# Kernel optimization log

Measured on AMD Instinct MI355X. Metric: run time of the kernel, lower is better.

Reference implementation:

```python
import jax, jax.numpy as jnp
import numpy as np

NEG_SLOPE = 0.01  # torch LeakyReLU default
MIN_FREQ = 1.0
MAX_FREQ = 10.0
W = 100
N_HIDDEN = 100
N_OBS = 64

def _leaky(x):
    return jnp.where(x >= 0, x, NEG_SLOPE * x)

def setup_inputs() -> dict:
    key = jax.random.key(0)
    ks = jax.random.split(key, 7)
    # kaiming_uniform-ish init scales (exact init doesn't matter for correctness baseline)
    def unif(k, shape, fan_in):
        bound = np.sqrt(6.0 / fan_in)
        return jax.random.uniform(k, shape, jnp.float32, -bound, bound)
    x = jax.random.normal(ks[0], (65536, N_OBS), jnp.float32)
    W_in = unif(ks[1], (N_OBS, W), N_OBS)
    b_in = jnp.zeros((W,), jnp.float32)
    Ws = unif(ks[2], (N_HIDDEN, W, W), W)
    bs = jnp.zeros((N_HIDDEN, W), jnp.float32)
    W_out = unif(ks[3], (W, 1), W)
    b_out = jnp.zeros((1,), jnp.float32)
    return {"x": x, "W_in": W_in, "b_in": b_in, "Ws": Ws, "bs": bs,
            "W_out": W_out, "b_out": b_out}

def reference(x, W_in, b_in, Ws, bs, W_out, b_out):
    h = _leaky(x @ W_in + b_in)                       # [B, 100]
    def layer(h, wb):
        w, b = wb
        return _leaky(h @ w + b), None
    h, _ = jax.lax.scan(layer, h, (Ws, bs))           # 100 hidden layers
    a = h @ W_out + b_out                             # [B, 1]
    a = jnp.tanh(a)
    return (a + 1.0) / 2.0 * (MAX_FREQ - MIN_FREQ) + MIN_FREQ
```

## Files before the change

kernel.cpp:

```cpp
#include <hip/hip_runtime.h>
#include <cmath>

#define NLAYERS 100
#define DIN     64
#define WDIM    100
#define NTT     4
#define RT      2
#define ROWS    64
#define WAVES   2
#define BROWS   (WAVES * ROWS)
#define KS      7
#define FRAGS   (KS * NTT)
#define FPW     (FRAGS / WAVES)

typedef _Float16 half8  __attribute__((ext_vector_type(8)));
typedef _Float16 half2v __attribute__((ext_vector_type(2)));
typedef __fp16   fp16x2 __attribute__((ext_vector_type(2)));
typedef float    f32x4  __attribute__((ext_vector_type(4)));
typedef float    f32x16 __attribute__((ext_vector_type(16)));
typedef unsigned uint4v __attribute__((ext_vector_type(4)));

#define WSH_LAYER_HALVES (KS * NTT * 64 * 8)
#define WSH_HALVES       (NLAYERS * WSH_LAYER_HALVES)
#define W0_HALVES        (4 * NTT * 64 * 8)
#define BPAD_FLOATS      128
#define OFF_BPAD_B       ((WSH_HALVES + W0_HALVES) * 2)
#define OFF_WOUT_B       (OFF_BPAD_B + BPAD_FLOATS * 4)
#define WOUT_FLOATS      128

__global__ __launch_bounds__(256)
void actor_prep(const float* __restrict__ Win, const float* __restrict__ bin,
                const float* __restrict__ Ws,  const float* __restrict__ bs,
                const float* __restrict__ Wout,
                _Float16* __restrict__ wsh, _Float16* __restrict__ w0sh,
                float* __restrict__ bpad, float* __restrict__ woutp) {
    __shared__ float tile[16 * 128];
    const int bid = blockIdx.x, tid = threadIdx.x;
    if (bid < NLAYERS * KS) {
        const int l = bid / KS, ks = bid % KS;
#pragma unroll
        for (int e = 0; e < 8; ++e) {
            int idx = tid + 256 * e;
            int kk = idx >> 7, nn = idx & 127;
            int k = ks * 16 + kk;
            float v = 0.f;
            if (k < WDIM && nn < WDIM)        v = Ws[(l * WDIM + k) * WDIM + nn];
            else if (k == WDIM && nn < WDIM)  v = bs[l * WDIM + nn];
            else if (k == WDIM && nn == WDIM) v = 1.0f;
            tile[idx] = v;
        }
        __syncthreads();
        const int lane = tid & 63, nt = tid >> 6;
        const int g = lane >> 5, n = nt * 32 + (lane & 31);
        half8 o;
#pragma unroll
        for (int j = 0; j < 8; ++j) o[j] = (_Float16)tile[(g * 8 + j) * 128 + n];
        *(half8*)(wsh + (((l * KS + ks) * NTT + nt) << 9) + lane * 8) = o;
        return;
    }
    int b2 = bid - NLAYERS * KS;
    if (b2 < 4) {
        const int ks = b2;
#pragma unroll
        for (int e = 0; e < 8; ++e) {
            int idx = tid + 256 * e;
            int kk = idx >> 7, nn = idx & 127;
            int k = ks * 16 + kk;
            tile[idx] = (nn < WDIM) ? Win[k * WDIM + nn] : 0.f;
        }
        __syncthreads();
        const int lane = tid & 63, nt = tid >> 6;
        const int g = lane >> 5, n = nt * 32 + (lane & 31);
        half8 o;
#pragma unroll
        for (int j = 0; j < 8; ++j) o[j] = (_Float16)tile[(g * 8 + j) * 128 + n];
        *(half8*)(w0sh + ((ks * NTT + nt) << 9) + lane * 8) = o;
        return;
    }
    if (tid < BPAD_FLOATS) {
        bpad[tid] = (tid < WDIM) ? bin[tid] : (tid == WDIM ? 1.0f : 0.f);
    } else {
        int t = tid - BPAD_FLOATS;
        if (t < WOUT_FLOATS) woutp[t] = (t < WDIM) ? Wout[t] : 0.f;
    }
}

__device__ __forceinline__ void stage16(const _Float16* __restrict__ g,
                                        _Float16* l) {
    __builtin_amdgcn_global_load_lds(
        (const __attribute__((address_space(1))) unsigned*)g,
        (__attribute__((address_space(3))) unsigned*)l, 16, 0, 0);
}

__device__ __forceinline__ void split8(const float* __restrict__ p, half8& hi, half8& lo) {
    f32x4 u0 = *(const f32x4*)p;
    f32x4 u1 = *(const f32x4*)(p + 4);
    float v[8] = {u0[0], u0[1], u0[2], u0[3], u1[0], u1[1], u1[2], u1[3]};
#pragma unroll
    for (int e = 0; e < 8; e += 2) {
        fp16x2 h = __builtin_amdgcn_cvt_pkrtz(v[e], v[e + 1]);
        float r0 = v[e]     - (float)h[0];
        float r1 = v[e + 1] - (float)h[1];
        fp16x2 l = __builtin_amdgcn_cvt_pkrtz(r0, r1);
        hi[e] = (_Float16)h[0]; hi[e + 1] = (_Float16)h[1];
        lo[e] = (_Float16)l[0]; lo[e + 1] = (_Float16)l[1];
    }
}

__device__ __forceinline__ unsigned pack2(float a, float b) {
    half2v p; p[0] = (_Float16)a; p[1] = (_Float16)b;
    const half2v slope = {(_Float16)0.01f, (_Float16)0.01f};
    p = __builtin_elementwise_max(p, p * slope);
    return __builtin_bit_cast(unsigned, p);
}

__device__ __forceinline__ void pack_bh(const f32x16 (&acc)[RT][NTT], half8 (&bh)[RT][KS]) {
#pragma unroll
    for (int rt = 0; rt < RT; ++rt)
#pragma unroll
        for (int ks = 0; ks < KS; ++ks) {
            const int r0 = 8 * (ks & 1);
            const f32x16 a = acc[rt][ks >> 1];
            unsigned lo0 = pack2(a[r0 + 0], a[r0 + 1]);
            unsigned lo1 = pack2(a[r0 + 2], a[r0 + 3]);
            unsigned hi0 = pack2(a[r0 + 4], a[r0 + 5]);
            unsigned hi1 = pack2(a[r0 + 6], a[r0 + 7]);
            asm volatile("v_permlane32_swap_b32 %0, %1" : "+v"(lo0), "+v"(hi0));
            asm volatile("v_permlane32_swap_b32 %0, %1" : "+v"(lo1), "+v"(hi1));
            uint4v u = {lo0, lo1, hi0, hi1};
            bh[rt][ks] = __builtin_bit_cast(half8, u);
        }
}

static __device__ const f32x16 kZero16 = {0,0,0,0, 0,0,0,0, 0,0,0,0, 0,0,0,0};

__global__ __launch_bounds__(128, 2)
void actor_main(const float* __restrict__ x,
                const _Float16* __restrict__ wsh,
                const _Float16* __restrict__ w0sh,
                const float* __restrict__ bpad,
                const float* __restrict__ woutp,
                const float* __restrict__ bout,
                float* __restrict__ out) {
    __shared__ __align__(16) _Float16 wlds[2 * WSH_LAYER_HALVES];
    const int tid  = threadIdx.x;
    const int lane = tid & 63;
    const int wid  = tid >> 6;
    const int g = lane >> 5, b31 = lane & 31;
    const int rowbase = blockIdx.x * BROWS + wid * ROWS;

    f32x16 acc[RT][NTT];
    half8 bh[RT][KS];
    half8 wreg[3][NTT];

#pragma unroll
    for (int f = 0; f < FPW; ++f) {
        const int fr = wid * FPW + f;
        stage16(wsh + fr * 512 + lane * 8, wlds + fr * 512);
    }

    {
        half8 w0[4][NTT];
#pragma unroll
        for (int ks = 0; ks < 4; ++ks)
#pragma unroll
            for (int nt = 0; nt < NTT; ++nt)
                w0[ks][nt] = *(const half8*)(w0sh + (ks * NTT + nt) * 512 + lane * 8);
#pragma unroll
        for (int rt = 0; rt < RT; ++rt)
#pragma unroll
            for (int nt = 0; nt < NTT; ++nt)
#pragma unroll
                for (int qd = 0; qd < 4; ++qd) {
                    f32x4 tq = *(const f32x4*)(bpad + nt * 32 + 8 * qd + 4 * g);
#pragma unroll
                    for (int r = 0; r < 4; ++r) acc[rt][nt][4 * qd + r] = tq[r];
                }
#pragma unroll
        for (int rt = 0; rt < RT; ++rt) {
            const float* xr = x + (rowbase + rt * 32 + b31) * DIN;
#pragma unroll
            for (int ks = 0; ks < 4; ++ks) {
                half8 xhi, xlo;
                split8(xr + ks * 16 + g * 8, xhi, xlo);
#pragma unroll
                for (int nt = 0; nt < NTT; ++nt) {
                    acc[rt][nt] = __builtin_amdgcn_mfma_f32_32x32x16_f16(w0[ks][nt], xhi, acc[rt][nt], 0, 0, 0);
                    acc[rt][nt] = __builtin_amdgcn_mfma_f32_32x32x16_f16(w0[ks][nt], xlo, acc[rt][nt], 0, 0, 0);
                }
            }
        }
    }
    pack_bh(acc, bh);
    __syncthreads();

#pragma unroll 1
    for (int l = 0; l < NLAYERS; ++l) {
        const _Float16* rb = wlds + (l & 1) * WSH_LAYER_HALVES;
        _Float16* sb = wlds + ((l + 1) & 1) * WSH_LAYER_HALVES;
        const int ln = (l + 1 < NLAYERS) ? l + 1 : NLAYERS - 1;
        const _Float16* wn = wsh + ln * WSH_LAYER_HALVES;

#pragma unroll
        for (int f = 0; f < FPW; ++f) {
            const int fr = wid * FPW + f;
            stage16(wn + fr * 512 + lane * 8, sb + fr * 512);
        }
#pragma unroll
        for (int kp = 0; kp < 2; ++kp)
#pragma unroll
            for (int nt = 0; nt < NTT; ++nt)
                wreg[kp][nt] = *(const half8*)(rb + (kp * NTT + nt) * 512 + lane * 8);
#pragma unroll
        for (int ks = 0; ks < KS; ++ks) {
            const int s = ks % 3;
#pragma unroll
            for (int rt = 0; rt < RT; ++rt)
#pragma unroll
                for (int nt = 0; nt < NTT; ++nt)
                    acc[rt][nt] = __builtin_amdgcn_mfma_f32_32x32x16_f16(
                        wreg[s][nt], bh[rt][ks], (ks == 0 ? kZero16 : acc[rt][nt]), 0, 0, 0);
            if (ks + 2 < KS) {
                const int s2 = (ks + 2) % 3;
#pragma unroll
                for (int nt = 0; nt < NTT; ++nt)
                    wreg[s2][nt] = *(const half8*)(rb + ((ks + 2) * NTT + nt) * 512 + lane * 8);
            }
        }
        if (l < NLAYERS - 1)
            pack_bh(acc, bh);
        __syncthreads();
    }

    float part[RT];
#pragma unroll
    for (int rt = 0; rt < RT; ++rt) {
        float s = 0.f;
#pragma unroll
        for (int nt = 0; nt < NTT; ++nt)
#pragma unroll
            for (int qd = 0; qd < 4; ++qd) {
                f32x4 w4 = *(const f32x4*)(woutp + nt * 32 + 8 * qd + 4 * g);
#pragma unroll
                for (int r = 0; r < 4; ++r) {
                    float a = acc[rt][nt][4 * qd + r];
                    float v = fmaxf(a, 0.01f * a);
                    s += v * w4[r];
                }
            }
        s += __shfl_xor(s, 32);
        part[rt] = s;
    }
    if (lane < 32) {
#pragma unroll
        for (int rt = 0; rt < RT; ++rt) {
            float tot = part[rt] + bout[0];
            out[rowbase + rt * 32 + b31] = tanhf(tot) * 4.5f + 5.5f;
        }
    }
}

extern "C" void kernel_launch(void* const* d_in, const int* in_sizes, int n_in,
                              void* d_out, int out_size, void* d_ws, size_t ws_size,
                              hipStream_t stream) {
    const float* x    = (const float*)d_in[0];
    const float* Win  = (const float*)d_in[1];
    const float* bin  = (const float*)d_in[2];
    const float* Ws   = (const float*)d_in[3];
    const float* bs   = (const float*)d_in[4];
    const float* Wout = (const float*)d_in[5];
    const float* bout = (const float*)d_in[6];
    float* out = (float*)d_out;

    char* ws = (char*)d_ws;
    _Float16* wsh  = (_Float16*)ws;
    _Float16* w0sh = wsh + WSH_HALVES;
    float* bpad  = (float*)(ws + OFF_BPAD_B);
    float* woutp = (float*)(ws + OFF_WOUT_B);

    hipLaunchKernelGGL(actor_prep, dim3(NLAYERS * KS + 4 + 1), dim3(256), 0, stream,
                       Win, bin, Ws, bs, Wout, wsh, w0sh, bpad, woutp);

    const int nrows = in_sizes[0] / DIN;
    hipLaunchKernelGGL(actor_main, dim3(nrows / BROWS), dim3(WAVES * 64), 0, stream,
                       x, wsh, w0sh, bpad, woutp, bout, out);
}
```

Measured before the change: 263.7 us.

## Use four waves of 32 rows each and load full layer weights upfront

Each wave now handles 32 rows instead of 64 (one row tile), and each block has 4 waves instead of 2. Block rows stay at 128, and per-layer LDS weight staging is spread over 4 waves. Per layer, all 28 weight fragments are read from LDS into registers before the MFMAs run, replacing the rolling 3-slot prefetch. The aim is more waves per CU to hide latency and cheaper per-wave LDS staging. In exchange, the LDS weight reads are amortised over half as many MFMAs per wave, and the larger register buffer may limit occupancy.

```diff
diff --git a/kernel.cpp b/kernel.cpp
--- a/kernel.cpp
+++ b/kernel.cpp
@@ -5,9 +5,8 @@
 #define DIN     64
 #define WDIM    100
 #define NTT     4
-#define RT      2
-#define ROWS    64
-#define WAVES   2
+#define ROWS    32
+#define WAVES   4
 #define BROWS   (WAVES * ROWS)
 #define KS      7
 #define FRAGS   (KS * NTT)
@@ -114,27 +113,25 @@
     return __builtin_bit_cast(unsigned, p);
 }
 
-__device__ __forceinline__ void pack_bh(const f32x16 (&acc)[RT][NTT], half8 (&bh)[RT][KS]) {
-#pragma unroll
-    for (int rt = 0; rt < RT; ++rt)
-#pragma unroll
-        for (int ks = 0; ks < KS; ++ks) {
-            const int r0 = 8 * (ks & 1);
-            const f32x16 a = acc[rt][ks >> 1];
-            unsigned lo0 = pack2(a[r0 + 0], a[r0 + 1]);
-            unsigned lo1 = pack2(a[r0 + 2], a[r0 + 3]);
-            unsigned hi0 = pack2(a[r0 + 4], a[r0 + 5]);
-            unsigned hi1 = pack2(a[r0 + 6], a[r0 + 7]);
-            asm volatile("v_permlane32_swap_b32 %0, %1" : "+v"(lo0), "+v"(hi0));
-            asm volatile("v_permlane32_swap_b32 %0, %1" : "+v"(lo1), "+v"(hi1));
-            uint4v u = {lo0, lo1, hi0, hi1};
-            bh[rt][ks] = __builtin_bit_cast(half8, u);
-        }
+__device__ __forceinline__ void pack_bh(const f32x16 (&acc)[NTT], half8 (&bh)[KS]) {
+#pragma unroll
+    for (int ks = 0; ks < KS; ++ks) {
+        const int r0 = 8 * (ks & 1);
+        const f32x16 a = acc[ks >> 1];
+        unsigned lo0 = pack2(a[r0 + 0], a[r0 + 1]);
+        unsigned lo1 = pack2(a[r0 + 2], a[r0 + 3]);
+        unsigned hi0 = pack2(a[r0 + 4], a[r0 + 5]);
+        unsigned hi1 = pack2(a[r0 + 6], a[r0 + 7]);
+        asm volatile("v_permlane32_swap_b32 %0, %1" : "+v"(lo0), "+v"(hi0));
+        asm volatile("v_permlane32_swap_b32 %0, %1" : "+v"(lo1), "+v"(hi1));
+        uint4v u = {lo0, lo1, hi0, hi1};
+        bh[ks] = __builtin_bit_cast(half8, u);
+    }
 }
 
 static __device__ const f32x16 kZero16 = {0,0,0,0, 0,0,0,0, 0,0,0,0, 0,0,0,0};
 
-__global__ __launch_bounds__(128, 2)
+__global__ __launch_bounds__(256, 2)
 void actor_main(const float* __restrict__ x,
                 const _Float16* __restrict__ wsh,
                 const _Float16* __restrict__ w0sh,
@@ -149,9 +146,9 @@
     const int g = lane >> 5, b31 = lane & 31;
     const int rowbase = blockIdx.x * BROWS + wid * ROWS;
 
-    f32x16 acc[RT][NTT];
-    half8 bh[RT][KS];
-    half8 wreg[3][NTT];
+    f32x16 acc[NTT];
+    half8 bh[KS];
+    half8 wb[KS][NTT];
 
 #pragma unroll
     for (int f = 0; f < FPW; ++f) {
@@ -167,27 +164,22 @@
             for (int nt = 0; nt < NTT; ++nt)
                 w0[ks][nt] = *(const half8*)(w0sh + (ks * NTT + nt) * 512 + lane * 8);
 #pragma unroll
-        for (int rt = 0; rt < RT; ++rt)
-#pragma unroll
-            for (int nt = 0; nt < NTT; ++nt)
-#pragma unroll
-                for (int qd = 0; qd < 4; ++qd) {
-                    f32x4 tq = *(const f32x4*)(bpad + nt * 32 + 8 * qd + 4 * g);
-#pragma unroll
-                    for (int r = 0; r < 4; ++r) acc[rt][nt][4 * qd + r] = tq[r];
-                }
-#pragma unroll
-        for (int rt = 0; rt < RT; ++rt) {
-            const float* xr = x + (rowbase + rt * 32 + b31) * DIN;
-#pragma unroll
-            for (int ks = 0; ks < 4; ++ks) {
-                half8 xhi, xlo;
-                split8(xr + ks * 16 + g * 8, xhi, xlo);
-#pragma unroll
-                for (int nt = 0; nt < NTT; ++nt) {
-                    acc[rt][nt] = __builtin_amdgcn_mfma_f32_32x32x16_f16(w0[ks][nt], xhi, acc[rt][nt], 0, 0, 0);
-                    acc[rt][nt] = __builtin_amdgcn_mfma_f32_32x32x16_f16(w0[ks][nt], xlo, acc[rt][nt], 0, 0, 0);
-                }
+        for (int nt = 0; nt < NTT; ++nt)
+#pragma unroll
+            for (int qd = 0; qd < 4; ++qd) {
+                f32x4 tq = *(const f32x4*)(bpad + nt * 32 + 8 * qd + 4 * g);
+#pragma unroll
+                for (int r = 0; r < 4; ++r) acc[nt][4 * qd + r] = tq[r];
+            }
+        const float* xr = x + (rowbase + b31) * DIN;
+#pragma unroll
+        for (int ks = 0; ks < 4; ++ks) {
+            half8 xhi, xlo;
+            split8(xr + ks * 16 + g * 8, xhi, xlo);
+#pragma unroll
+            for (int nt = 0; nt < NTT; ++nt) {
+                acc[nt] = __builtin_amdgcn_mfma_f32_32x32x16_f16(w0[ks][nt], xhi, acc[nt], 0, 0, 0);
+                acc[nt] = __builtin_amdgcn_mfma_f32_32x32x16_f16(w0[ks][nt], xlo, acc[nt], 0, 0, 0);
             }
         }
     }
@@ -207,56 +199,38 @@
             stage16(wn + fr * 512 + lane * 8, sb + fr * 512);
         }
 #pragma unroll
-        for (int kp = 0; kp < 2; ++kp)
+        for (int ks = 0; ks < KS; ++ks)
 #pragma unroll
             for (int nt = 0; nt < NTT; ++nt)
-                wreg[kp][nt] = *(const half8*)(rb + (kp * NTT + nt) * 512 + lane * 8);
-#pragma unroll
-        for (int ks = 0; ks < KS; ++ks) {
-            const int s = ks % 3;
-#pragma unroll
-            for (int rt = 0; rt < RT; ++rt)
-#pragma unroll
-                for (int nt = 0; nt < NTT; ++nt)
-                    acc[rt][nt] = __builtin_amdgcn_mfma_f32_32x32x16_f16(
-                        wreg[s][nt], bh[rt][ks], (ks == 0 ? kZero16 : acc[rt][nt]), 0, 0, 0);
-            if (ks + 2 < KS) {
-                const int s2 = (ks + 2) % 3;
-#pragma unroll
-                for (int nt = 0; nt < NTT; ++nt)
-                    wreg[s2][nt] = *(const half8*)(rb + ((ks + 2) * NTT + nt) * 512 + lane * 8);
-            }
-        }
+                wb[ks][nt] = *(const half8*)(rb + (ks * NTT + nt) * 512 + lane * 8);
+#pragma unroll
+        for (int ks = 0; ks < KS; ++ks)
+#pragma unroll
+            for (int nt = 0; nt < NTT; ++nt)
+                acc[nt] = __builtin_amdgcn_mfma_f32_32x32x16_f16(
+                    wb[ks][nt], bh[ks], (ks == 0 ? kZero16 : acc[nt]), 0, 0, 0);
         if (l < NLAYERS - 1)
             pack_bh(acc, bh);
         __syncthreads();
     }
 
-    float part[RT];
-#pragma unroll
-    for (int rt = 0; rt < RT; ++rt) {
-        float s = 0.f;
-#pragma unroll
-        for (int nt = 0; nt < NTT; ++nt)
-#pragma unroll
-            for (int qd = 0; qd < 4; ++qd) {
-                f32x4 w4 = *(const f32x4*)(woutp + nt * 32 + 8 * qd + 4 * g);
-#pragma unroll
-                for (int r = 0; r < 4; ++r) {
-                    float a = acc[rt][nt][4 * qd + r];
-                    float v = fmaxf(a, 0.01f * a);
-                    s += v * w4[r];
-                }
+    float s = 0.f;
+#pragma unroll
+    for (int nt = 0; nt < NTT; ++nt)
+#pragma unroll
+        for (int qd = 0; qd < 4; ++qd) {
+            f32x4 w4 = *(const f32x4*)(woutp + nt * 32 + 8 * qd + 4 * g);
+#pragma unroll
+            for (int r = 0; r < 4; ++r) {
+                float a = acc[nt][4 * qd + r];
+                float v = fmaxf(a, 0.01f * a);
+                s += v * w4[r];
             }
-        s += __shfl_xor(s, 32);
-        part[rt] = s;
-    }
+        }
+    s += __shfl_xor(s, 32);
     if (lane < 32) {
-#pragma unroll
-        for (int rt = 0; rt < RT; ++rt) {
-            float tot = part[rt] + bout[0];
-            out[rowbase + rt * 32 + b31] = tanhf(tot) * 4.5f + 5.5f;
-        }
+        float tot = s + bout[0];
+        out[rowbase + b31] = tanhf(tot) * 4.5f + 5.5f;
     }
 }
 
```

New measurement: 245.1 us (median of 2 runs). 1.08x faster.
